# Performance work log

Hardware: AMD Instinct MI355X
Metric: run time of the kernel (lower is better)

The kernel has to match this reference:

```python
import jax, jax.numpy as jnp
import numpy as np

N_NODES = 100000


def _gcn_norm(edge_index, num_nodes):
    # PyG GCNConv default: add self-loops, symmetric normalization
    src, dst = edge_index[0], edge_index[1]
    loop = jnp.arange(num_nodes, dtype=src.dtype)
    src = jnp.concatenate([src, loop])
    dst = jnp.concatenate([dst, loop])
    deg = jax.ops.segment_sum(jnp.ones_like(dst, dtype=jnp.float32), dst,
                              num_segments=num_nodes)
    dinv = jnp.where(deg > 0, jax.lax.rsqrt(deg), 0.0)
    norm = dinv[src] * dinv[dst]  # [E + N]
    return src, dst, norm


def _gcn_conv(x, W, b, src, dst, norm, num_nodes):
    h = x @ W                                   # [N, out] linear first (PyG)
    msg = h[src] * norm[:, None]                # gather + scale  [E+N, out]
    out = jax.ops.segment_sum(msg, dst, num_segments=num_nodes)  # scatter-add
    return out + b


def setup_inputs() -> dict:
    key = jax.random.key(0)
    ks = jax.random.split(key, 5)
    x = jax.random.normal(ks[0], (N_NODES, 3), dtype=jnp.float32)
    edge_index = jax.random.randint(ks[1], (2, 1600000), 0, N_NODES, dtype=jnp.int64)
    # Glorot-ish weights, zero bias (PyG defaults)
    W1 = jax.random.normal(ks[2], (3, 64), dtype=jnp.float32) * (1.0 / np.sqrt(3))
    W2 = jax.random.normal(ks[3], (64, 64), dtype=jnp.float32) * (1.0 / np.sqrt(64))
    W3 = jax.random.normal(ks[4], (64, 3), dtype=jnp.float32) * (1.0 / np.sqrt(64))
    b1 = jnp.zeros((64,), jnp.float32)
    b2 = jnp.zeros((64,), jnp.float32)
    b3 = jnp.zeros((3,), jnp.float32)
    return {"x": x, "edge_index": edge_index, "W1": W1, "b1": b1,
            "W2": W2, "b2": b2, "W3": W3, "b3": b3}


def reference(x, edge_index, W1, b1, W2, b2, W3, b3):
    n = x.shape[0]
    src, dst, norm = _gcn_norm(edge_index, n)  # same graph for every layer
    h = jax.nn.relu(_gcn_conv(x, W1, b1, src, dst, norm, n))
    h = jax.nn.relu(_gcn_conv(h, W2, b2, src, dst, norm, n))
    return _gcn_conv(h, W3, b3, src, dst, norm, n)
```

## Files before the change

kernel.cpp:

```cpp
#include <hip/hip_runtime.h>

#define TPB 256
#define NB 391
#define CH 8192
#define BS 4736


__device__ __forceinline__ unsigned bpack(float a, float b) {
    unsigned ua = __float_as_uint(a), ub = __float_as_uint(b);
    ua = (ua + 0x7fffu + ((ua >> 16) & 1u)) >> 16;
    ub = (ub + 0x7fffu + ((ub >> 16) & 1u)) >> 16;
    return ua | (ub << 16);
}
__device__ __forceinline__ float blo(unsigned u) { return __uint_as_float(u << 16); }
__device__ __forceinline__ float bhi(unsigned u) { return __uint_as_float(u & 0xffff0000u); }


__global__ __launch_bounds__(512) void k_init(unsigned* __restrict__ gcur) {
    int t = threadIdx.x;
    if (t < NB) gcur[t] = (unsigned)(t * BS);
}


__global__ __launch_bounds__(TPB) void k_placeA(const int* __restrict__ src,
                                                const int* __restrict__ dst,
                                                unsigned* __restrict__ gcur,
                                                unsigned* __restrict__ bkt, int E) {
    __shared__ unsigned val[CH];
    __shared__ unsigned short bid[CH];
    __shared__ unsigned cnt[512], loff[512], lcur[512], basev[512];
    __shared__ unsigned tsum[TPB];
    int t = threadIdx.x;
    int c0 = blockIdx.x * CH;
    int n = E - c0; if (n > CH) n = CH;

    for (int b = t; b < 512; b += TPB) { cnt[b] = 0; lcur[b] = 0; }
    __syncthreads();
    for (int i = t; i < n; i += TPB)
        atomicAdd(&cnt[(unsigned)dst[c0 + i] >> 8], 1u);
    __syncthreads();
    for (int b = t; b < NB; b += TPB)
        basev[b] = cnt[b] ? atomicAdd(&gcur[b], cnt[b]) : 0u;
    unsigned a0 = cnt[2 * t], a1 = cnt[2 * t + 1];
    tsum[t] = a0 + a1;
    __syncthreads();
#pragma unroll
    for (int o = 1; o < TPB; o <<= 1) {
        unsigned v = (t >= o) ? tsum[t - o] : 0u;
        __syncthreads();
        tsum[t] += v;
        __syncthreads();
    }
    unsigned ex = tsum[t] - (a0 + a1);
    loff[2 * t] = ex; loff[2 * t + 1] = ex + a0;
    __syncthreads();
    for (int i = t; i < n; i += TPB) {
        unsigned s = (unsigned)src[c0 + i];
        unsigned d = (unsigned)dst[c0 + i];
        unsigned b = d >> 8;
        unsigned r = atomicAdd(&lcur[b], 1u);
        unsigned slot = loff[b] + r;
        val[slot] = s | ((d & 255u) << 20);
        bid[slot] = (unsigned short)b;
    }
    __syncthreads();
    for (int i = t; i < n; i += TPB) {
        unsigned b = bid[i];
        bkt[basev[b] + ((unsigned)i - loff[b])] = val[i];
    }
}


__global__ __launch_bounds__(TPB) void k_fineS(const unsigned* __restrict__ bkt,
                                               const unsigned* __restrict__ gcur,
                                               const float* __restrict__ x,
                                               int2* __restrict__ rp2,
                                               int* __restrict__ ssrc,
                                               float* __restrict__ dinv,
                                               float4* __restrict__ xs4, int N) {
    __shared__ unsigned cnt[256], sc[256], off[256];
    int t = threadIdx.x, b = blockIdx.x;
    cnt[t] = 0;
    __syncthreads();
    int p0 = b * BS, p1 = (int)gcur[b];
    for (int i = p0 + t; i < p1; i += TPB)
        atomicAdd(&cnt[bkt[i] >> 20], 1u);
    __syncthreads();
    unsigned c = cnt[t];
    sc[t] = c;
    __syncthreads();
#pragma unroll
    for (int o = 1; o < 256; o <<= 1) {
        unsigned v = (t >= o) ? sc[t - o] : 0u;
        __syncthreads();
        sc[t] += v;
        __syncthreads();
    }
    unsigned ex = sc[t] - c;
    off[t] = (unsigned)p0 + ex;
    int node = (b << 8) + t;
    if (node < N) {
        int beg = p0 + (int)ex;
        rp2[node] = make_int2(beg, beg + (int)c);
        float dv = rsqrtf((float)(c + 1u));
        dinv[node] = dv;
        float4 xv;
        xv.x = x[node * 3 + 0] * dv;
        xv.y = x[node * 3 + 1] * dv;
        xv.z = x[node * 3 + 2] * dv;
        xv.w = 0.f;
        xs4[node] = xv;
    }
    __syncthreads();
    for (int i = p0 + t; i < p1; i += TPB) {
        unsigned u = bkt[i];
        unsigned r = atomicAdd(&off[u >> 20], 1u);
        ssrc[r] = (int)(u & 0xFFFFFu);
    }
}


__global__ __launch_bounds__(TPB) void k_l1q(const float* __restrict__ xs4,
                                             const int2* __restrict__ rp2,
                                             const int* __restrict__ ssrc,
                                             const float* __restrict__ dinv,
                                             const float* __restrict__ W1,
                                             const float* __restrict__ b1,
                                             const float* __restrict__ W2,
                                             uint4* __restrict__ gb, int N) {
    __shared__ float Ws[4096];
    for (int i = threadIdx.x; i < 4096; i += TPB) Ws[i] = W2[i];
    __syncthreads();
    int tid = blockIdx.x * TPB + threadIdx.x;
    int node = tid >> 2, c = tid & 3;
    if (node >= N) return;
    int2 r = rp2[node];
    float acc = xs4[tid];
    int j = r.x;
    for (; j + 3 < r.y; j += 4) {
        int s0 = ssrc[j], s1 = ssrc[j+1], s2 = ssrc[j+2], s3 = ssrc[j+3];
        acc += (xs4[(s0 << 2) + c] + xs4[(s1 << 2) + c])
             + (xs4[(s2 << 2) + c] + xs4[(s3 << 2) + c]);
    }
    for (; j < r.y; ++j) acc += xs4[(ssrc[j] << 2) + c];
    float dv = dinv[node];
    acc *= dv;
    int base = (threadIdx.x & 63) & ~3;
    float q0 = __shfl(acc, base + 0, 64);
    float q1 = __shfl(acc, base + 1, 64);
    float q2 = __shfl(acc, base + 2, 64);

    float o[16];
#pragma unroll
    for (int i = 0; i < 16; ++i) o[i] = 0.f;
    const int cofs = c << 4;
    for (int kb = 0; kb < 16; ++kb) {
        int k0 = __builtin_amdgcn_readfirstlane(kb) << 2;
        const float* W1k = W1 + k0;
        const float* b1k = b1 + k0;
        float h[4];
        h[0] = fmaxf(fmaf(q0, W1k[0], fmaf(q1, W1k[64], fmaf(q2, W1k[128], b1k[0]))), 0.f);
        h[1] = fmaxf(fmaf(q0, W1k[1], fmaf(q1, W1k[65], fmaf(q2, W1k[129], b1k[1]))), 0.f);
        h[2] = fmaxf(fmaf(q0, W1k[2], fmaf(q1, W1k[66], fmaf(q2, W1k[130], b1k[2]))), 0.f);
        h[3] = fmaxf(fmaf(q0, W1k[3], fmaf(q1, W1k[67], fmaf(q2, W1k[131], b1k[3]))), 0.f);
#pragma unroll
        for (int kk = 0; kk < 4; ++kk) {
            const float4* Wp = (const float4*)(Ws + ((k0 + kk) << 6) + cofs);
#pragma unroll
            for (int ii = 0; ii < 4; ++ii) {
                float4 w = Wp[ii];
                o[4*ii+0] = fmaf(h[kk], w.x, o[4*ii+0]);
                o[4*ii+1] = fmaf(h[kk], w.y, o[4*ii+1]);
                o[4*ii+2] = fmaf(h[kk], w.z, o[4*ii+2]);
                o[4*ii+3] = fmaf(h[kk], w.w, o[4*ii+3]);
            }
        }
    }
    uint4 v0, v1;
    v0.x = bpack(o[0] * dv,  o[1] * dv);
    v0.y = bpack(o[2] * dv,  o[3] * dv);
    v0.z = bpack(o[4] * dv,  o[5] * dv);
    v0.w = bpack(o[6] * dv,  o[7] * dv);
    v1.x = bpack(o[8] * dv,  o[9] * dv);
    v1.y = bpack(o[10] * dv, o[11] * dv);
    v1.z = bpack(o[12] * dv, o[13] * dv);
    v1.w = bpack(o[14] * dv, o[15] * dv);
    uint4* gp = gb + ((size_t)node << 3) + (c << 1);
    gp[0] = v0;
    gp[1] = v1;
}


__global__ __launch_bounds__(TPB) void k_p2fb(const uint4* __restrict__ gb,
                                              const int2* __restrict__ rp2,
                                              const int* __restrict__ ssrc,
                                              const float* __restrict__ dinv,
                                              const float* __restrict__ b2,
                                              const float* __restrict__ W3,
                                              float* __restrict__ q4, int N) {
    int tid = blockIdx.x * TPB + threadIdx.x;
    int node = tid >> 3, q = tid & 7;
    if (node >= N) return;
    int2 r = rp2[node];
    int beg = r.x, end = r.y;
    float a[8];
    {
        uint4 u = gb[((size_t)node << 3) + q];
        a[0] = blo(u.x); a[1] = bhi(u.x);
        a[2] = blo(u.y); a[3] = bhi(u.y);
        a[4] = blo(u.z); a[5] = bhi(u.z);
        a[6] = blo(u.w); a[7] = bhi(u.w);
    }
    int j = beg;
    for (; j + 3 < end; j += 4) {
        int s0 = ssrc[j], s1 = ssrc[j+1], s2 = ssrc[j+2], s3 = ssrc[j+3];
        uint4 u0 = gb[((size_t)s0 << 3) + q];
        uint4 u1 = gb[((size_t)s1 << 3) + q];
        uint4 u2 = gb[((size_t)s2 << 3) + q];
        uint4 u3 = gb[((size_t)s3 << 3) + q];
        a[0] += (blo(u0.x) + blo(u1.x)) + (blo(u2.x) + blo(u3.x));
        a[1] += (bhi(u0.x) + bhi(u1.x)) + (bhi(u2.x) + bhi(u3.x));
        a[2] += (blo(u0.y) + blo(u1.y)) + (blo(u2.y) + blo(u3.y));
        a[3] += (bhi(u0.y) + bhi(u1.y)) + (bhi(u2.y) + bhi(u3.y));
        a[4] += (blo(u0.z) + blo(u1.z)) + (blo(u2.z) + blo(u3.z));
        a[5] += (bhi(u0.z) + bhi(u1.z)) + (bhi(u2.z) + bhi(u3.z));
        a[6] += (blo(u0.w) + blo(u1.w)) + (blo(u2.w) + blo(u3.w));
        a[7] += (bhi(u0.w) + bhi(u1.w)) + (bhi(u2.w) + bhi(u3.w));
    }
    for (; j < end; ++j) {
        uint4 u = gb[((size_t)ssrc[j] << 3) + q];
        a[0] += blo(u.x); a[1] += bhi(u.x);
        a[2] += blo(u.y); a[3] += bhi(u.y);
        a[4] += blo(u.z); a[5] += bhi(u.z);
        a[6] += blo(u.w); a[7] += bhi(u.w);
    }
    float dv = dinv[node];
    int f0 = q << 3;
    const float* bb = b2 + f0;
    const float* Wr = W3 + f0 * 3;
    float p0 = 0.f, p1 = 0.f, p2 = 0.f;
#pragma unroll
    for (int i = 0; i < 8; ++i) {
        float h = fmaxf(fmaf(a[i], dv, bb[i]), 0.f);
        p0 = fmaf(h, Wr[3*i+0], p0);
        p1 = fmaf(h, Wr[3*i+1], p1);
        p2 = fmaf(h, Wr[3*i+2], p2);
    }
#pragma unroll
    for (int off = 1; off < 8; off <<= 1) {
        p0 += __shfl_xor(p0, off, 64);
        p1 += __shfl_xor(p1, off, 64);
        p2 += __shfl_xor(p2, off, 64);
    }
    if (q < 4) {
        float v = (q == 0) ? p0 * dv : (q == 1) ? p1 * dv : (q == 2) ? p2 * dv : 0.f;
        q4[((size_t)node << 2) + q] = v;
    }
}


__global__ __launch_bounds__(TPB) void k_pull3o(const float* __restrict__ g34,
                                                const int2* __restrict__ rp2,
                                                const int* __restrict__ ssrc,
                                                const float* __restrict__ dinv,
                                                const float* __restrict__ b3,
                                                float* __restrict__ out, int N) {
    int tid = blockIdx.x * TPB + threadIdx.x;
    int node = tid >> 2, c = tid & 3;
    if (node >= N) return;
    int2 r = rp2[node];
    int beg = r.x, end = r.y;
    float acc = g34[tid];
    int j = beg;
    for (; j + 3 < end; j += 4) {
        int s0 = ssrc[j], s1 = ssrc[j+1], s2 = ssrc[j+2], s3 = ssrc[j+3];
        acc += (g34[(s0 << 2) + c] + g34[(s1 << 2) + c])
             + (g34[(s2 << 2) + c] + g34[(s3 << 2) + c]);
    }
    for (; j < end; ++j) acc += g34[(ssrc[j] << 2) + c];
    if (c < 3) out[(size_t)node * 3 + c] = dinv[node] * acc + b3[c];
}

extern "C" void kernel_launch(void* const* d_in, const int* in_sizes, int n_in,
                              void* d_out, int out_size, void* d_ws, size_t ws_size,
                              hipStream_t stream) {
    const float* x  = (const float*)d_in[0];
    const int*   ei = (const int*)  d_in[1];
    const float* W1 = (const float*)d_in[2];
    const float* b1 = (const float*)d_in[3];
    const float* W2 = (const float*)d_in[4];
    const float* b2 = (const float*)d_in[5];
    const float* W3 = (const float*)d_in[6];
    const float* b3 = (const float*)d_in[7];
    float* out = (float*)d_out;

    const int N = in_sizes[0] / 3;
    const int E = in_sizes[1] / 2;
    const int* srcI = ei;
    const int* dstI = ei + E;

    float*    ws   = (float*)d_ws;
    unsigned* gcur = (unsigned*)ws;
    int2*     rp2  = (int2*)    (ws + 512);
    float*    dinv = ws + 512 + 2 * (size_t)N;
    int*      ssrc = (int*)     (dinv + N);
    float*    xs4  = (float*)(ssrc + (size_t)NB * BS + 4);
    float*    q4   = xs4 + (size_t)N * 4;
    unsigned* gb   = (unsigned*)(q4 + (size_t)N * 4);
    unsigned* bkt  = gb + (size_t)N * 32;

    int gPlace = (E + CH - 1) / CH;
    int gS3    = (N * 4 + TPB - 1) / TPB;
    int gP2    = (int)(((size_t)N * 8 + TPB - 1) / TPB);

    k_init  <<<1,      512, 0, stream>>>(gcur);
    k_placeA<<<gPlace, TPB, 0, stream>>>(srcI, dstI, gcur, bkt, E);
    k_fineS <<<NB,     TPB, 0, stream>>>(bkt, gcur, x, rp2, ssrc, dinv,
                                         (float4*)xs4, N);

    k_l1q<<<gS3, TPB, 0, stream>>>(xs4, rp2, ssrc, dinv,
                                   W1, b1, W2, (uint4*)gb, N);

    k_p2fb<<<gP2, TPB, 0, stream>>>((const uint4*)gb, rp2, ssrc, dinv,
                                    b2, W3, q4, N);

    k_pull3o<<<gS3, TPB, 0, stream>>>(q4, rp2, ssrc, dinv, b3, out, N);
}
```

Baseline: 211.3 us.

## Split layer-2 gather into two feature-half passes over a split bf16 layout

The bf16 layer-2 features are stored as two separate planes of 32 features each, one per half. The layer-2 aggregation now runs as two launches, each gathering 64-byte rows from a half-size table and accumulating its partial layer-3 projection into q4. The aim is better cache locality for the random gather, since each pass touches half the footprint, at the cost of reading the CSR indices twice and a read-modify-write of q4. The placement chunk is also halved and the fine-sort kernel uses 512 threads per block.

```diff
diff --git a/kernel.cpp b/kernel.cpp
--- a/kernel.cpp
+++ b/kernel.cpp
@@ -2,7 +2,7 @@
 
 #define TPB 256
 #define NB 391
-#define CH 8192
+#define CH 4096
 #define BS 4736
 
 
@@ -71,7 +71,7 @@
 }
 
 
-__global__ __launch_bounds__(TPB) void k_fineS(const unsigned* __restrict__ bkt,
+__global__ __launch_bounds__(512) void k_fineS(const unsigned* __restrict__ bkt,
                                                const unsigned* __restrict__ gcur,
                                                const float* __restrict__ x,
                                                int2* __restrict__ rp2,
@@ -80,39 +80,41 @@
                                                float4* __restrict__ xs4, int N) {
     __shared__ unsigned cnt[256], sc[256], off[256];
     int t = threadIdx.x, b = blockIdx.x;
-    cnt[t] = 0;
+    if (t < 256) cnt[t] = 0;
     __syncthreads();
     int p0 = b * BS, p1 = (int)gcur[b];
-    for (int i = p0 + t; i < p1; i += TPB)
+    for (int i = p0 + t; i < p1; i += 512)
         atomicAdd(&cnt[bkt[i] >> 20], 1u);
     __syncthreads();
-    unsigned c = cnt[t];
-    sc[t] = c;
+    unsigned c = (t < 256) ? cnt[t] : 0u;
+    if (t < 256) sc[t] = c;
     __syncthreads();
 #pragma unroll
     for (int o = 1; o < 256; o <<= 1) {
-        unsigned v = (t >= o) ? sc[t - o] : 0u;
+        unsigned v = (t >= o && t < 256) ? sc[t - o] : 0u;
         __syncthreads();
-        sc[t] += v;
+        if (t < 256) sc[t] += v;
         __syncthreads();
     }
-    unsigned ex = sc[t] - c;
-    off[t] = (unsigned)p0 + ex;
-    int node = (b << 8) + t;
-    if (node < N) {
-        int beg = p0 + (int)ex;
-        rp2[node] = make_int2(beg, beg + (int)c);
-        float dv = rsqrtf((float)(c + 1u));
-        dinv[node] = dv;
-        float4 xv;
-        xv.x = x[node * 3 + 0] * dv;
-        xv.y = x[node * 3 + 1] * dv;
-        xv.z = x[node * 3 + 2] * dv;
-        xv.w = 0.f;
-        xs4[node] = xv;
-    }
-    __syncthreads();
-    for (int i = p0 + t; i < p1; i += TPB) {
+    if (t < 256) {
+        unsigned ex = sc[t] - c;
+        off[t] = (unsigned)p0 + ex;
+        int node = (b << 8) + t;
+        if (node < N) {
+            int beg = p0 + (int)ex;
+            rp2[node] = make_int2(beg, beg + (int)c);
+            float dv = rsqrtf((float)(c + 1u));
+            dinv[node] = dv;
+            float4 xv;
+            xv.x = x[node * 3 + 0] * dv;
+            xv.y = x[node * 3 + 1] * dv;
+            xv.z = x[node * 3 + 2] * dv;
+            xv.w = 0.f;
+            xs4[node] = xv;
+        }
+    }
+    __syncthreads();
+    for (int i = p0 + t; i < p1; i += 512) {
         unsigned u = bkt[i];
         unsigned r = atomicAdd(&off[u >> 20], 1u);
         ssrc[r] = (int)(u & 0xFFFFFu);
@@ -185,27 +187,28 @@
     v1.y = bpack(o[10] * dv, o[11] * dv);
     v1.z = bpack(o[12] * dv, o[13] * dv);
     v1.w = bpack(o[14] * dv, o[15] * dv);
-    uint4* gp = gb + ((size_t)node << 3) + (c << 1);
+    uint4* gp = gb + ((size_t)(c >> 1) * N << 2) + ((size_t)node << 2) + ((c & 1) << 1);
     gp[0] = v0;
     gp[1] = v1;
 }
 
 
-__global__ __launch_bounds__(TPB) void k_p2fb(const uint4* __restrict__ gb,
+__global__ __launch_bounds__(TPB) void k_p2fb(const uint4* __restrict__ gbr,
                                               const int2* __restrict__ rp2,
                                               const int* __restrict__ ssrc,
                                               const float* __restrict__ dinv,
                                               const float* __restrict__ b2,
                                               const float* __restrict__ W3,
-                                              float* __restrict__ q4, int N) {
+                                              float* __restrict__ q4,
+                                              int N, int pass) {
     int tid = blockIdx.x * TPB + threadIdx.x;
-    int node = tid >> 3, q = tid & 7;
+    int node = tid >> 2, q = tid & 3;
     if (node >= N) return;
     int2 r = rp2[node];
     int beg = r.x, end = r.y;
     float a[8];
     {
-        uint4 u = gb[((size_t)node << 3) + q];
+        uint4 u = gbr[((size_t)node << 2) + q];
         a[0] = blo(u.x); a[1] = bhi(u.x);
         a[2] = blo(u.y); a[3] = bhi(u.y);
         a[4] = blo(u.z); a[5] = bhi(u.z);
@@ -214,10 +217,10 @@
     int j = beg;
     for (; j + 3 < end; j += 4) {
         int s0 = ssrc[j], s1 = ssrc[j+1], s2 = ssrc[j+2], s3 = ssrc[j+3];
-        uint4 u0 = gb[((size_t)s0 << 3) + q];
-        uint4 u1 = gb[((size_t)s1 << 3) + q];
-        uint4 u2 = gb[((size_t)s2 << 3) + q];
-        uint4 u3 = gb[((size_t)s3 << 3) + q];
+        uint4 u0 = gbr[((size_t)s0 << 2) + q];
+        uint4 u1 = gbr[((size_t)s1 << 2) + q];
+        uint4 u2 = gbr[((size_t)s2 << 2) + q];
+        uint4 u3 = gbr[((size_t)s3 << 2) + q];
         a[0] += (blo(u0.x) + blo(u1.x)) + (blo(u2.x) + blo(u3.x));
         a[1] += (bhi(u0.x) + bhi(u1.x)) + (bhi(u2.x) + bhi(u3.x));
         a[2] += (blo(u0.y) + blo(u1.y)) + (blo(u2.y) + blo(u3.y));
@@ -228,14 +231,14 @@
         a[7] += (bhi(u0.w) + bhi(u1.w)) + (bhi(u2.w) + bhi(u3.w));
     }
     for (; j < end; ++j) {
-        uint4 u = gb[((size_t)ssrc[j] << 3) + q];
+        uint4 u = gbr[((size_t)ssrc[j] << 2) + q];
         a[0] += blo(u.x); a[1] += bhi(u.x);
         a[2] += blo(u.y); a[3] += bhi(u.y);
         a[4] += blo(u.z); a[5] += bhi(u.z);
         a[6] += blo(u.w); a[7] += bhi(u.w);
     }
     float dv = dinv[node];
-    int f0 = q << 3;
+    int f0 = (pass << 5) + (q << 3);
     const float* bb = b2 + f0;
     const float* Wr = W3 + f0 * 3;
     float p0 = 0.f, p1 = 0.f, p2 = 0.f;
@@ -246,16 +249,16 @@
         p1 = fmaf(h, Wr[3*i+1], p1);
         p2 = fmaf(h, Wr[3*i+2], p2);
     }
-#pragma unroll
-    for (int off = 1; off < 8; off <<= 1) {
-        p0 += __shfl_xor(p0, off, 64);
-        p1 += __shfl_xor(p1, off, 64);
-        p2 += __shfl_xor(p2, off, 64);
-    }
-    if (q < 4) {
-        float v = (q == 0) ? p0 * dv : (q == 1) ? p1 * dv : (q == 2) ? p2 * dv : 0.f;
-        q4[((size_t)node << 2) + q] = v;
-    }
+    p0 += __shfl_xor(p0, 1, 64);
+    p1 += __shfl_xor(p1, 1, 64);
+    p2 += __shfl_xor(p2, 1, 64);
+    p0 += __shfl_xor(p0, 2, 64);
+    p1 += __shfl_xor(p1, 2, 64);
+    p2 += __shfl_xor(p2, 2, 64);
+    float v = (q == 0) ? p0 * dv : (q == 1) ? p1 * dv : (q == 2) ? p2 * dv : 0.f;
+    size_t oi = ((size_t)node << 2) + q;
+    if (pass == 0) q4[oi] = v;
+    else           q4[oi] += v;
 }
 
 
@@ -311,18 +314,19 @@
 
     int gPlace = (E + CH - 1) / CH;
     int gS3    = (N * 4 + TPB - 1) / TPB;
-    int gP2    = (int)(((size_t)N * 8 + TPB - 1) / TPB);
 
     k_init  <<<1,      512, 0, stream>>>(gcur);
     k_placeA<<<gPlace, TPB, 0, stream>>>(srcI, dstI, gcur, bkt, E);
-    k_fineS <<<NB,     TPB, 0, stream>>>(bkt, gcur, x, rp2, ssrc, dinv,
+    k_fineS <<<NB,     512, 0, stream>>>(bkt, gcur, x, rp2, ssrc, dinv,
                                          (float4*)xs4, N);
 
     k_l1q<<<gS3, TPB, 0, stream>>>(xs4, rp2, ssrc, dinv,
                                    W1, b1, W2, (uint4*)gb, N);
 
-    k_p2fb<<<gP2, TPB, 0, stream>>>((const uint4*)gb, rp2, ssrc, dinv,
-                                    b2, W3, q4, N);
+    k_p2fb<<<gS3, TPB, 0, stream>>>((const uint4*)gb, rp2, ssrc, dinv,
+                                    b2, W3, q4, N, 0);
+    k_p2fb<<<gS3, TPB, 0, stream>>>((const uint4*)(gb + (size_t)N * 16), rp2, ssrc,
+                                    dinv, b2, W3, q4, N, 1);
 
     k_pull3o<<<gS3, TPB, 0, stream>>>(q4, rp2, ssrc, dinv, b3, out, N);
 }
```

Result: no change. 215.5 us (+2.0%).

## Cache bucket and dst values in LDS, halve placement chunk, widen fine-sort blocks

Applied to the files above, without the earlier changes.

k_placeA now stores dst values in shared memory on its first pass so the second pass does not reload them from global memory. The chunk size is halved, giving more blocks and keeping LDS usage within limits. k_fineS caches its bucket slice in shared memory, so the scatter pass no longer re-reads global memory, and it runs 512 threads per block for more parallelism. The cost is more LDS per block and more global atomics on gcur, since there are more chunks.

```diff
diff --git a/kernel.cpp b/kernel.cpp
--- a/kernel.cpp
+++ b/kernel.cpp
@@ -2,7 +2,7 @@
 
 #define TPB 256
 #define NB 391
-#define CH 8192
+#define CH 4096
 #define BS 4736
 
 
@@ -27,6 +27,7 @@
                                                 unsigned* __restrict__ gcur,
                                                 unsigned* __restrict__ bkt, int E) {
     __shared__ unsigned val[CH];
+    __shared__ unsigned dstS[CH];
     __shared__ unsigned short bid[CH];
     __shared__ unsigned cnt[512], loff[512], lcur[512], basev[512];
     __shared__ unsigned tsum[TPB];
@@ -36,8 +37,11 @@
 
     for (int b = t; b < 512; b += TPB) { cnt[b] = 0; lcur[b] = 0; }
     __syncthreads();
-    for (int i = t; i < n; i += TPB)
-        atomicAdd(&cnt[(unsigned)dst[c0 + i] >> 8], 1u);
+    for (int i = t; i < n; i += TPB) {
+        unsigned d = (unsigned)dst[c0 + i];
+        dstS[i] = d;
+        atomicAdd(&cnt[d >> 8], 1u);
+    }
     __syncthreads();
     for (int b = t; b < NB; b += TPB)
         basev[b] = cnt[b] ? atomicAdd(&gcur[b], cnt[b]) : 0u;
@@ -56,7 +60,7 @@
     __syncthreads();
     for (int i = t; i < n; i += TPB) {
         unsigned s = (unsigned)src[c0 + i];
-        unsigned d = (unsigned)dst[c0 + i];
+        unsigned d = dstS[i];
         unsigned b = d >> 8;
         unsigned r = atomicAdd(&lcur[b], 1u);
         unsigned slot = loff[b] + r;
@@ -71,7 +75,7 @@
 }
 
 
-__global__ __launch_bounds__(TPB) void k_fineS(const unsigned* __restrict__ bkt,
+__global__ __launch_bounds__(512) void k_fineS(const unsigned* __restrict__ bkt,
                                                const unsigned* __restrict__ gcur,
                                                const float* __restrict__ x,
                                                int2* __restrict__ rp2,
@@ -79,41 +83,48 @@
                                                float* __restrict__ dinv,
                                                float4* __restrict__ xs4, int N) {
     __shared__ unsigned cnt[256], sc[256], off[256];
+    __shared__ unsigned bs[BS];
     int t = threadIdx.x, b = blockIdx.x;
-    cnt[t] = 0;
+    if (t < 256) cnt[t] = 0;
     __syncthreads();
     int p0 = b * BS, p1 = (int)gcur[b];
-    for (int i = p0 + t; i < p1; i += TPB)
-        atomicAdd(&cnt[bkt[i] >> 20], 1u);
-    __syncthreads();
-    unsigned c = cnt[t];
-    sc[t] = c;
+    int n = p1 - p0;
+    for (int i = t; i < n; i += 512) {
+        unsigned u = bkt[p0 + i];
+        bs[i] = u;
+        atomicAdd(&cnt[u >> 20], 1u);
+    }
+    __syncthreads();
+    unsigned c = (t < 256) ? cnt[t] : 0u;
+    if (t < 256) sc[t] = c;
     __syncthreads();
 #pragma unroll
     for (int o = 1; o < 256; o <<= 1) {
-        unsigned v = (t >= o) ? sc[t - o] : 0u;
+        unsigned v = (t >= o && t < 256) ? sc[t - o] : 0u;
         __syncthreads();
-        sc[t] += v;
+        if (t < 256) sc[t] += v;
         __syncthreads();
     }
-    unsigned ex = sc[t] - c;
-    off[t] = (unsigned)p0 + ex;
-    int node = (b << 8) + t;
-    if (node < N) {
-        int beg = p0 + (int)ex;
-        rp2[node] = make_int2(beg, beg + (int)c);
-        float dv = rsqrtf((float)(c + 1u));
-        dinv[node] = dv;
-        float4 xv;
-        xv.x = x[node * 3 + 0] * dv;
-        xv.y = x[node * 3 + 1] * dv;
-        xv.z = x[node * 3 + 2] * dv;
-        xv.w = 0.f;
-        xs4[node] = xv;
-    }
-    __syncthreads();
-    for (int i = p0 + t; i < p1; i += TPB) {
-        unsigned u = bkt[i];
+    if (t < 256) {
+        unsigned ex = sc[t] - c;
+        off[t] = (unsigned)p0 + ex;
+        int node = (b << 8) + t;
+        if (node < N) {
+            int beg = p0 + (int)ex;
+            rp2[node] = make_int2(beg, beg + (int)c);
+            float dv = rsqrtf((float)(c + 1u));
+            dinv[node] = dv;
+            float4 xv;
+            xv.x = x[node * 3 + 0] * dv;
+            xv.y = x[node * 3 + 1] * dv;
+            xv.z = x[node * 3 + 2] * dv;
+            xv.w = 0.f;
+            xs4[node] = xv;
+        }
+    }
+    __syncthreads();
+    for (int i = t; i < n; i += 512) {
+        unsigned u = bs[i];
         unsigned r = atomicAdd(&off[u >> 20], 1u);
         ssrc[r] = (int)(u & 0xFFFFFu);
     }
@@ -315,7 +326,7 @@
 
     k_init  <<<1,      512, 0, stream>>>(gcur);
     k_placeA<<<gPlace, TPB, 0, stream>>>(srcI, dstI, gcur, bkt, E);
-    k_fineS <<<NB,     TPB, 0, stream>>>(bkt, gcur, x, rp2, ssrc, dinv,
+    k_fineS <<<NB,     512, 0, stream>>>(bkt, gcur, x, rp2, ssrc, dinv,
                                          (float4*)xs4, N);
 
     k_l1q<<<gS3, TPB, 0, stream>>>(xs4, rp2, ssrc, dinv,
```

Result: no change. 208.9 us (-1.1%).
